# Optimization experiments

Measured on AMD Instinct MI355X. Metric: run time of the kernel, lower is better.

## Reference

```python
import jax, jax.numpy as jnp
import numpy as np
from functools import partial


def _givens_indices(nDims):
    tops, btms = [], []
    for iTop in range(nDims - 1):
        for iBtm in range(iTop + 1, nDims):
            tops.append(iTop)
            btms.append(iBtm)
    return jnp.asarray(tops, dtype=jnp.int32), jnp.asarray(btms, dtype=jnp.int32)


def _orthmtxgen(angles):
    # angles: [M, nAngles]; nAngles = nDims*(nDims-1)/2
    M, nAng = angles.shape
    nDims = int((1 + np.sqrt(1 + 8 * nAng)) / 2)
    tops, btms = _givens_indices(nDims)
    mat0 = jnp.broadcast_to(jnp.eye(nDims, dtype=angles.dtype), (M, nDims, nDims))

    def step(mat, inp):
        t, b, a = inp               # t,b scalar int32; a: [M]
        a = a[:, None]              # [M,1]
        c = jnp.cos(a)
        s = jnp.sin(a)
        vt = jax.lax.dynamic_index_in_dim(mat, t, axis=1, keepdims=False)  # [M,nDims]
        vb = jax.lax.dynamic_index_in_dim(mat, b, axis=1, keepdims=False)
        # exact 3-multiply Givens update as in the torch source
        u = s * (vt + vb)
        vt_new = (c + s) * vt - u
        vb_new = (c - s) * vb + u
        mat = jax.lax.dynamic_update_index_in_dim(mat, vb_new, b, axis=1)
        mat = jax.lax.dynamic_update_index_in_dim(mat, vt_new, t, axis=1)
        return mat, None

    mat, _ = jax.lax.scan(step, mat0, (tops, btms, angles.T))
    return mat


def setup_inputs() -> dict:
    key = jax.random.key(0)
    k1, k2 = jax.random.split(key)
    M, nDims, nSamples = 1024, 32, 2048
    nAngles = nDims * (nDims - 1) // 2  # 496
    x = jax.random.normal(k1, (M, nDims, nSamples), dtype=jnp.float32)
    angles = jax.random.normal(k2, (M, nAngles), dtype=jnp.float32)
    mus = jnp.ones((M, nDims), dtype=jnp.float32)
    return {"x": x, "angles": angles, "mus": mus}


def reference(x, angles, mus):
    # R = diag(mus) applied row-wise to the product of Givens rotations
    R = mus[:, :, None] * _orthmtxgen(angles)   # [M,nDims,nDims]
    return jnp.matmul(R, x)                      # Analysis mode: R @ x
```

## Files before the change

kernel.cpp:

```cpp
#include <hip/hip_runtime.h>
#include <math.h>

#define NDIMS 32
#define NANG 496
#define MPB 4
#define TCOLS 128

typedef float f32x4 __attribute__((ext_vector_type(4)));
typedef float f32x2 __attribute__((ext_vector_type(2)));

__device__ __forceinline__ void load16_to_lds(const float* gsrc, float* ldst) {
    __builtin_amdgcn_global_load_lds(
        (const __attribute__((address_space(1))) void*)gsrc,
        (__attribute__((address_space(3))) void*)ldst,
        16, 0, 0);
}

__global__ __launch_bounds__(128)
void gen_R(const float* __restrict__ angles, const float* __restrict__ mus,
           float* __restrict__ RT)
{
    __shared__ float2 cs[MPB][NANG];
    const int tid = threadIdx.x;
    const int m0  = blockIdx.x * MPB;

    for (int idx = tid; idx < MPB * NANG; idx += 128) {
        const int lm = idx / NANG, a = idx - lm * NANG;
        float sv, cv;
        sincosf(angles[(size_t)(m0 + lm) * NANG + a], &sv, &cv);
        cs[lm][a] = make_float2(cv, sv);
    }
    __syncthreads();

    const int lm = tid >> 5, j = tid & 31;
    const int m  = m0 + lm;

    float r[NDIMS];
    #pragma unroll
    for (int i = 0; i < NDIMS; ++i) r[i] = (i == j) ? 1.0f : 0.0f;

    int sidx = 0;
    #pragma unroll
    for (int t = 0; t < NDIMS - 1; ++t) {
        #pragma unroll
        for (int b = t + 1; b < NDIMS; ++b) {
            const float2 v = cs[lm][sidx]; ++sidx;
            const float c = v.x, sn = v.y;
            const float vt = r[t], vb = r[b];
            const float u  = sn * (vt + vb);
            r[t] = (c + sn) * vt - u;
            r[b] = (c - sn) * vb + u;
        }
    }

    float* dst = RT + (size_t)m * (NDIMS * NDIMS) + (size_t)j * NDIMS;
    const float* mu = mus + (size_t)m * NDIMS;
    #pragma unroll
    for (int i = 0; i < NDIMS; i += 4) {
        f32x4 v;
        v.x = r[i + 0] * mu[i + 0];
        v.y = r[i + 1] * mu[i + 1];
        v.z = r[i + 2] * mu[i + 2];
        v.w = r[i + 3] * mu[i + 3];
        *reinterpret_cast<f32x4*>(dst + i) = v;
    }
}

__global__ __launch_bounds__(256, 8)
void apply_T2(const float* __restrict__ x, const float* __restrict__ RT,
              float* __restrict__ out, int S)
{
    __shared__ float rt[NDIMS * NDIMS];
    __shared__ float xt[NDIMS][TCOLS];

    const int tid  = threadIdx.x;
    const int m    = blockIdx.x;
    const int wid  = tid >> 6;
    const int lane = tid & 63;
    const int col0 = blockIdx.y * TCOLS;

    const float* __restrict__ xm = x   + (size_t)m * NDIMS * S + col0;
    float*       __restrict__ om = out + (size_t)m * NDIMS * S + col0;

    load16_to_lds(RT + (size_t)m * (NDIMS * NDIMS) + wid * 256 + lane * 4,
                  &rt[wid * 256]);

    const size_t srcRow = (size_t)(lane >> 5) * S + (lane & 31) * 4;
    #pragma unroll
    for (int p = 0; p < 4; ++p) {
        const int k = wid * 8 + p * 2;
        load16_to_lds(xm + (size_t)k * S + srcRow, &xt[k][0]);
    }
    __syncthreads();

    const int i0 = wid * 8;

    f32x2 acc[8];
    #pragma unroll
    for (int r = 0; r < 8; ++r) acc[r] = (f32x2)0.0f;

    #pragma unroll 2
    for (int k = 0; k < NDIMS; ++k) {
        const f32x2 xv = *reinterpret_cast<const f32x2*>(&xt[k][lane * 2]);
        const f32x4 ra = *reinterpret_cast<const f32x4*>(&rt[k * NDIMS + i0]);
        const f32x4 rb = *reinterpret_cast<const f32x4*>(&rt[k * NDIMS + i0 + 4]);
        acc[0] += ra.x * xv;
        acc[1] += ra.y * xv;
        acc[2] += ra.z * xv;
        acc[3] += ra.w * xv;
        acc[4] += rb.x * xv;
        acc[5] += rb.y * xv;
        acc[6] += rb.z * xv;
        acc[7] += rb.w * xv;
    }

    #pragma unroll
    for (int r = 0; r < 8; ++r)
        __builtin_nontemporal_store(acc[r],
            reinterpret_cast<f32x2*>(om + (size_t)(i0 + r) * S + lane * 2));
}

#define RT_STRIDE 36
__global__ __launch_bounds__(256, 4)
void soot_fused(const float* __restrict__ x, const float* __restrict__ angles,
                const float* __restrict__ mus, float* __restrict__ out, int S)
{
    __shared__ float2 cs[NANG];
    __shared__ float  RT[NDIMS * RT_STRIDE];
    const int tid = threadIdx.x;
    const int m   = blockIdx.x;

    for (int s0 = tid; s0 < NANG; s0 += 256) {
        float sv, cv;
        sincosf(angles[(size_t)m * NANG + s0], &sv, &cv);
        cs[s0] = make_float2(cv, sv);
    }
    __syncthreads();

    if (tid < NDIMS) {
        const int j = tid;
        float r[NDIMS];
        #pragma unroll
        for (int i = 0; i < NDIMS; ++i) r[i] = (i == j) ? 1.0f : 0.0f;
        int sidx = 0;
        #pragma unroll
        for (int t = 0; t < NDIMS - 1; ++t)
            #pragma unroll
            for (int b = t + 1; b < NDIMS; ++b) {
                const float2 v = cs[sidx]; ++sidx;
                const float c = v.x, sn = v.y;
                const float vt = r[t], vb = r[b];
                const float u  = sn * (vt + vb);
                r[t] = (c + sn) * vt - u;
                r[b] = (c - sn) * vb + u;
            }
        #pragma unroll
        for (int i = 0; i < NDIMS; ++i)
            RT[j * RT_STRIDE + i] = r[i] * mus[(size_t)m * NDIMS + i];
    }
    __syncthreads();

    for (int c0 = tid; c0 < S; c0 += 256) {
        float acc[NDIMS];
        #pragma unroll
        for (int i = 0; i < NDIMS; ++i) acc[i] = 0.f;
        #pragma unroll
        for (int k = 0; k < NDIMS; ++k) {
            const float xv = x[(size_t)m * NDIMS * S + (size_t)k * S + c0];
            #pragma unroll
            for (int i = 0; i < NDIMS; ++i)
                acc[i] = fmaf(RT[k * RT_STRIDE + i], xv, acc[i]);
        }
        #pragma unroll
        for (int i = 0; i < NDIMS; ++i)
            out[(size_t)m * NDIMS * S + (size_t)i * S + c0] = acc[i];
    }
}

extern "C" void kernel_launch(void* const* d_in, const int* in_sizes, int n_in,
                              void* d_out, int out_size, void* d_ws, size_t ws_size,
                              hipStream_t stream) {
    const float* x      = (const float*)d_in[0];
    const float* angles = (const float*)d_in[1];
    const float* mus    = (const float*)d_in[2];
    float* out          = (float*)d_out;

    const int M = in_sizes[1] / NANG;
    const int S = in_sizes[0] / (M * NDIMS);

    const size_t rt_bytes = (size_t)M * NDIMS * NDIMS * sizeof(float);
    if (ws_size >= rt_bytes && (M % MPB) == 0 && (S % TCOLS) == 0) {
        float* RT = (float*)d_ws;
        gen_R<<<dim3(M / MPB), 128, 0, stream>>>(angles, mus, RT);
        dim3 grid(M, S / TCOLS);
        apply_T2<<<grid, 256, 0, stream>>>(x, RT, out, S);
    } else {
        soot_fused<<<dim3(M), 256, 0, stream>>>(x, angles, mus, out, S);
    }
}
```

Measured before the change: 114.5 us.

## Make apply kernel persistent per matrix with double-buffered LDS prefetch

Replaces the 2D grid of one-tile blocks with one block per matrix that loops over all column tiles. The next x tile is prefetched into a second LDS buffer with async global-to-LDS loads while the current tile is computed, synchronised by manual vmcnt waits and barriers. This removes repeated RT loads and block launch overhead and overlaps loads with compute. In exchange the grid shrinks to M blocks, which reduces parallelism. The hand-counted vmcnt values must match the outstanding loads exactly, including the nontemporal stores, or the waits will be wrong.

```diff
diff --git a/kernel.cpp b/kernel.cpp
--- a/kernel.cpp
+++ b/kernel.cpp
@@ -66,21 +66,20 @@
     }
 }
 
-__global__ __launch_bounds__(256, 8)
-void apply_T2(const float* __restrict__ x, const float* __restrict__ RT,
+__global__ __launch_bounds__(256, 4)
+void apply_P1(const float* __restrict__ x, const float* __restrict__ RT,
               float* __restrict__ out, int S)
 {
     __shared__ float rt[NDIMS * NDIMS];
-    __shared__ float xt[NDIMS][TCOLS];
+    __shared__ float xt[2][NDIMS][TCOLS];
 
     const int tid  = threadIdx.x;
     const int m    = blockIdx.x;
     const int wid  = tid >> 6;
     const int lane = tid & 63;
-    const int col0 = blockIdx.y * TCOLS;
-
-    const float* __restrict__ xm = x   + (size_t)m * NDIMS * S + col0;
-    float*       __restrict__ om = out + (size_t)m * NDIMS * S + col0;
+
+    const float* __restrict__ xm = x   + (size_t)m * NDIMS * S;
+    float*       __restrict__ om = out + (size_t)m * NDIMS * S;
 
     load16_to_lds(RT + (size_t)m * (NDIMS * NDIMS) + wid * 256 + lane * 4,
                   &rt[wid * 256]);
@@ -89,35 +88,59 @@
     #pragma unroll
     for (int p = 0; p < 4; ++p) {
         const int k = wid * 8 + p * 2;
-        load16_to_lds(xm + (size_t)k * S + srcRow, &xt[k][0]);
-    }
-    __syncthreads();
+        load16_to_lds(xm + (size_t)k * S + srcRow, &xt[0][k][0]);
+    }
 
     const int i0 = wid * 8;
-
-    f32x2 acc[8];
-    #pragma unroll
-    for (int r = 0; r < 8; ++r) acc[r] = (f32x2)0.0f;
-
-    #pragma unroll 2
-    for (int k = 0; k < NDIMS; ++k) {
-        const f32x2 xv = *reinterpret_cast<const f32x2*>(&xt[k][lane * 2]);
-        const f32x4 ra = *reinterpret_cast<const f32x4*>(&rt[k * NDIMS + i0]);
-        const f32x4 rb = *reinterpret_cast<const f32x4*>(&rt[k * NDIMS + i0 + 4]);
-        acc[0] += ra.x * xv;
-        acc[1] += ra.y * xv;
-        acc[2] += ra.z * xv;
-        acc[3] += ra.w * xv;
-        acc[4] += rb.x * xv;
-        acc[5] += rb.y * xv;
-        acc[6] += rb.z * xv;
-        acc[7] += rb.w * xv;
-    }
-
-    #pragma unroll
-    for (int r = 0; r < 8; ++r)
-        __builtin_nontemporal_store(acc[r],
-            reinterpret_cast<f32x2*>(om + (size_t)(i0 + r) * S + lane * 2));
+    const int NT = S / TCOLS;
+
+    for (int t = 0; t < NT; ++t) {
+        const int cb = t & 1;
+
+        if (t + 1 < NT) {
+            const float* src = xm + (size_t)(t + 1) * TCOLS + srcRow;
+            #pragma unroll
+            for (int p = 0; p < 4; ++p) {
+                const int k = wid * 8 + p * 2;
+                load16_to_lds(src + (size_t)k * S, &xt[cb ^ 1][k][0]);
+            }
+            if (t == 0) {
+                asm volatile("s_waitcnt vmcnt(4)" ::: "memory");
+            } else {
+                asm volatile("s_waitcnt vmcnt(12)" ::: "memory");
+            }
+        } else {
+            asm volatile("s_waitcnt vmcnt(8)" ::: "memory");
+        }
+        __builtin_amdgcn_s_barrier();
+
+        f32x2 acc[8];
+        #pragma unroll
+        for (int r = 0; r < 8; ++r) acc[r] = (f32x2)0.0f;
+
+        #pragma unroll 2
+        for (int k = 0; k < NDIMS; ++k) {
+            const f32x2 xv = *reinterpret_cast<const f32x2*>(&xt[cb][k][lane * 2]);
+            const f32x4 ra = *reinterpret_cast<const f32x4*>(&rt[k * NDIMS + i0]);
+            const f32x4 rb = *reinterpret_cast<const f32x4*>(&rt[k * NDIMS + i0 + 4]);
+            acc[0] += ra.x * xv;
+            acc[1] += ra.y * xv;
+            acc[2] += ra.z * xv;
+            acc[3] += ra.w * xv;
+            acc[4] += rb.x * xv;
+            acc[5] += rb.y * xv;
+            acc[6] += rb.z * xv;
+            acc[7] += rb.w * xv;
+        }
+
+        float* ob = om + (size_t)t * TCOLS + lane * 2;
+        #pragma unroll
+        for (int r = 0; r < 8; ++r)
+            __builtin_nontemporal_store(acc[r],
+                reinterpret_cast<f32x2*>(ob + (size_t)(i0 + r) * S));
+
+        __builtin_amdgcn_s_barrier();
+    }
 }
 
 #define RT_STRIDE 36
@@ -189,11 +212,10 @@
     const int S = in_sizes[0] / (M * NDIMS);
 
     const size_t rt_bytes = (size_t)M * NDIMS * NDIMS * sizeof(float);
-    if (ws_size >= rt_bytes && (M % MPB) == 0 && (S % TCOLS) == 0) {
+    if (ws_size >= rt_bytes && (M % MPB) == 0 && (S % TCOLS) == 0 && S / TCOLS >= 2) {
         float* RT = (float*)d_ws;
         gen_R<<<dim3(M / MPB), 128, 0, stream>>>(angles, mus, RT);
-        dim3 grid(M, S / TCOLS);
-        apply_T2<<<grid, 256, 0, stream>>>(x, RT, out, S);
+        apply_P1<<<dim3(M), 256, 0, stream>>>(x, RT, out, S);
     } else {
         soot_fused<<<dim3(M), 256, 0, stream>>>(x, angles, mus, out, S);
     }
```

New measurement: 125.2 us. 1.09x slower.
